# Kernel optimization log

Measured on AMD Instinct MI355X. Metric: run time of the kernel, lower is better.

The kernel has to match this reference:

```python
import jax, jax.numpy as jnp
import numpy as np

B, H, W, C = 32, 224, 224, 3
HID = 64


def setup_inputs() -> dict:
    key = jax.random.key(0)
    k0, k1, k2 = jax.random.split(key, 3)
    inputs = jax.random.normal(k0, (B, H, W, C), dtype=jnp.float32)
    # Localization-net dense params. Original uses zeros init (identity transform);
    # we use small random weights plus the identity affine bias so the sampling
    # grid is a nontrivial perturbation of identity.
    w1 = jax.random.normal(k1, (H * W * C, HID), dtype=jnp.float32) * 1e-3
    b1 = jnp.zeros((HID,), dtype=jnp.float32)
    w2 = jax.random.normal(k2, (HID, 6), dtype=jnp.float32) * 1e-2
    b2 = jnp.array([1.0, 0.0, 0.0, 0.0, 1.0, 0.0], dtype=jnp.float32)
    return {"inputs": inputs, "w1": w1, "b1": b1, "w2": w2, "b2": b2}


def _bilinear_sampler(img, x_s, y_s):
    # img: [B,H,W,C]; x_s, y_s: [B,H,W] normalized coords in [-1,1]
    Bn, Hn, Wn, Cn = img.shape
    x = 0.5 * (x_s + 1.0) * (Wn - 1)
    y = 0.5 * (y_s + 1.0) * (Hn - 1)
    x0 = jnp.floor(x).astype(jnp.int32)
    x1 = x0 + 1
    y0 = jnp.floor(y).astype(jnp.int32)
    y1 = y0 + 1
    x0c = jnp.clip(x0, 0, Wn - 1)
    x1c = jnp.clip(x1, 0, Wn - 1)
    y0c = jnp.clip(y0, 0, Hn - 1)
    y1c = jnp.clip(y1, 0, Hn - 1)
    b_idx = jnp.arange(Bn, dtype=jnp.int32)[:, None, None]
    Ia = img[b_idx, y0c, x0c]  # [B,H,W,C]
    Ib = img[b_idx, y1c, x0c]
    Ic = img[b_idx, y0c, x1c]
    Id = img[b_idx, y1c, x1c]
    x0f = x0c.astype(x.dtype)
    x1f = x1c.astype(x.dtype)
    y0f = y0c.astype(y.dtype)
    y1f = y1c.astype(y.dtype)
    wa = ((x1f - x) * (y1f - y))[..., None]
    wb = ((x1f - x) * (y - y0f))[..., None]
    wc = ((x - x0f) * (y1f - y))[..., None]
    wd = ((x - x0f) * (y - y0f))[..., None]
    return wa * Ia + wb * Ib + wc * Ic + wd * Id


def reference(inputs, w1, b1, w2, b2):
    Bn, Hn, Wn, Cn = inputs.shape
    # NOTE: original keras code overwrites the conv branch with flatten(inputs),
    # so the conv/maxpool layers are dead code and omitted. Dropout is identity
    # at inference (training=False).
    flat = inputs.reshape(Bn, -1)
    h = jnp.tanh(flat @ w1 + b1)
    theta = jnp.tanh(h @ w2 + b2).reshape(Bn, 2, 3)
    # affine sampling grid over normalized target coords
    xt, yt = jnp.meshgrid(
        jnp.linspace(-1.0, 1.0, Wn, dtype=inputs.dtype),
        jnp.linspace(-1.0, 1.0, Hn, dtype=inputs.dtype),
    )  # each [H,W]
    grid = jnp.stack([xt.ravel(), yt.ravel(), jnp.ones_like(xt).ravel()])  # [3,H*W]
    batch_grid = jnp.einsum("bij,jk->bik", theta, grid).reshape(Bn, 2, Hn, Wn)
    x_s = batch_grid[:, 0]
    y_s = batch_grid[:, 1]
    return _bilinear_sampler(inputs, x_s, y_s)
```

## Files before the change

### kernel.cpp

```cpp
#include <hip/hip_runtime.h>

#define BATCH 32
#define HDIM 224
#define WDIM 224
#define CDIM 3
#define KTOT (HDIM * WDIM * CDIM)
#define HID 64
#define KCHUNK 256
#define NBLK1 (KTOT / KCHUNK)
#define PIX (HDIM * WDIM)
#define BLK3 49

__global__ __launch_bounds__(256, 4) void k1_gemm(const float* __restrict__ flat,
                                                  const float* __restrict__ w1,
                                                  float* __restrict__ part) {
    __shared__ float smem[8192];
    const int tid  = threadIdx.x;
    const int lane = tid & 63;
    const int wave = tid >> 6;
    const int k0   = blockIdx.x * KCHUNK;
    const int kw   = wave * 64;

    float w[64];
    const float* wp = w1 + (size_t)(k0 + kw) * HID + lane;
#pragma unroll
    for (int i = 0; i < 64; ++i)
        w[i] = wp[(size_t)i * HID];

#pragma unroll
    for (int t = 0; t < 8; ++t) {
        const int idx = tid + t * 256;
        const int b   = idx >> 6;
        const int kq  = idx & 63;
        *(float4*)(smem + b * 256 + kq * 4) =
            *(const float4*)(flat + (size_t)b * KTOT + k0 + kq * 4);
    }
    __syncthreads();

    float acc[32];
#pragma unroll
    for (int j = 0; j < 32; ++j) acc[j] = 0.0f;

#pragma unroll
    for (int kk = 0; kk < 64; kk += 4) {
#pragma unroll
        for (int b = 0; b < 32; ++b) {
            const float4 x = *(const float4*)(smem + b * 256 + kw + kk);
            float a = acc[b];
            a = fmaf(x.x, w[kk + 0], a);
            a = fmaf(x.y, w[kk + 1], a);
            a = fmaf(x.z, w[kk + 2], a);
            a = fmaf(x.w, w[kk + 3], a);
            acc[b] = a;
        }
    }
    __syncthreads();

#pragma unroll
    for (int j = 0; j < 32; ++j)
        smem[wave * 2048 + j * 64 + lane] = acc[j];
    __syncthreads();

    float* po = part + (size_t)blockIdx.x * 2048;
#pragma unroll
    for (int t = 0; t < 8; ++t) {
        const int idx = tid + t * 256;
        po[idx] = smem[idx] + smem[2048 + idx] +
                  smem[4096 + idx] + smem[6144 + idx];
    }
}

__global__ __launch_bounds__(256) void k1_reduce(const float* __restrict__ part,
                                                 float* __restrict__ hacc) {
    __shared__ float red[256];
    const int tid    = threadIdx.x;
    const int o      = tid & 31;
    const int g      = tid >> 5;
    const int o_base = blockIdx.x * 32;

    float s = 0.0f;
    for (int blk = g; blk < NBLK1; blk += 8)
        s += part[(size_t)blk * 2048 + o_base + o];
    red[tid] = s;
    __syncthreads();
    if (g == 0) {
        float t = 0.0f;
#pragma unroll
        for (int gg = 0; gg < 8; ++gg)
            t += red[gg * 32 + o];
        hacc[o_base + o] = t;
    }
}

__global__ __launch_bounds__(256) void k3_sample(const float* __restrict__ img,
                                                 const float* __restrict__ hacc,
                                                 const float* __restrict__ b1,
                                                 const float* __restrict__ w2,
                                                 const float* __restrict__ b2,
                                                 float* __restrict__ out) {
    const int b     = blockIdx.x / BLK3;
    const int strip = blockIdx.x - b * BLK3;
    const int tid   = threadIdx.x;

    __shared__ float sh[HID];
    __shared__ float sth[6];
    if (tid < HID)
        sh[tid] = tanhf(hacc[b * HID + tid] + b1[tid]);
    __syncthreads();
    if (tid < 6) {
        float s = b2[tid];
#pragma unroll
        for (int t = 0; t < HID; ++t)
            s = fmaf(sh[t], w2[t * 6 + tid], s);
        sth[tid] = tanhf(s);
    }
    __syncthreads();

    const float t0 = sth[0], t1 = sth[1], t2 = sth[2];
    const float t3 = sth[3], t4 = sth[4], t5 = sth[5];

    const float* base = img + (size_t)b * KTOT;
    const int pix0 = strip * 1024 + tid * 4;

    float res[12];
#pragma unroll
    for (int p = 0; p < 4; ++p) {
        const int pix = pix0 + p;
        const int i = pix / WDIM;
        const int j = pix - i * WDIM;

        const float xt = (2.0f * (float)j - (float)(WDIM - 1)) / (float)(WDIM - 1);
        const float yt = (2.0f * (float)i - (float)(HDIM - 1)) / (float)(HDIM - 1);

        const float xs = t0 * xt + t1 * yt + t2;
        const float ys = t3 * xt + t4 * yt + t5;

        const float x = 0.5f * (xs + 1.0f) * (float)(WDIM - 1);
        const float y = 0.5f * (ys + 1.0f) * (float)(HDIM - 1);

        const int x0 = (int)floorf(x);
        const int y0 = (int)floorf(y);

        const int x0c = min(max(x0, 0), WDIM - 1);
        const int x1c = min(max(x0 + 1, 0), WDIM - 1);
        const int y0c = min(max(y0, 0), HDIM - 1);
        const int y1c = min(max(y0 + 1, 0), HDIM - 1);

        const float x0f = (float)x0c, x1f = (float)x1c;
        const float y0f = (float)y0c, y1f = (float)y1c;

        const float wa = (x1f - x) * (y1f - y);
        const float wb = (x1f - x) * (y - y0f);
        const float wc = (x - x0f) * (y1f - y);
        const float wd = (x - x0f) * (y - y0f);

        const float* pa = base + (size_t)(y0c * WDIM + x0c) * 3;
        const float* pb = base + (size_t)(y1c * WDIM + x0c) * 3;
        const float* pc = base + (size_t)(y0c * WDIM + x1c) * 3;
        const float* pd = base + (size_t)(y1c * WDIM + x1c) * 3;

#pragma unroll
        for (int c = 0; c < 3; ++c)
            res[p * 3 + c] = wa * pa[c] + wb * pb[c] + wc * pc[c] + wd * pd[c];
    }

    float4* po = (float4*)(out + (size_t)b * KTOT + (size_t)pix0 * 3);
    po[0] = make_float4(res[0], res[1], res[2],  res[3]);
    po[1] = make_float4(res[4], res[5], res[6],  res[7]);
    po[2] = make_float4(res[8], res[9], res[10], res[11]);
}

extern "C" void kernel_launch(void* const* d_in, const int* in_sizes, int n_in,
                              void* d_out, int out_size, void* d_ws, size_t ws_size,
                              hipStream_t stream) {
    const float* inputs = (const float*)d_in[0];
    const float* w1     = (const float*)d_in[1];
    const float* b1     = (const float*)d_in[2];
    const float* w2     = (const float*)d_in[3];
    const float* b2     = (const float*)d_in[4];
    float* out = (float*)d_out;

    float* part = (float*)d_ws;
    float* hacc = part + (size_t)NBLK1 * 2048;

    k1_gemm<<<NBLK1, 256, 0, stream>>>(inputs, w1, part);
    k1_reduce<<<HID * BATCH / 32, 256, 0, stream>>>(part, hacc);
    k3_sample<<<BATCH * BLK3, 256, 0, stream>>>(inputs, hacc, b1, w2, b2, out);
}
```

Measured before the change: 152.1 us.

## Restructure localization GEMM into per-thread batch×hidden tiles with smaller K chunks

```diff
diff --git a/kernel.cpp b/kernel.cpp
--- a/kernel.cpp
+++ b/kernel.cpp
@@ -6,68 +6,73 @@
 #define CDIM 3
 #define KTOT (HDIM * WDIM * CDIM)
 #define HID 64
-#define KCHUNK 256
-#define NBLK1 (KTOT / KCHUNK)
+#define KC 128
+#define NBLK1 (KTOT / KC)
 #define PIX (HDIM * WDIM)
 #define BLK3 49
 
 __global__ __launch_bounds__(256, 4) void k1_gemm(const float* __restrict__ flat,
                                                   const float* __restrict__ w1,
                                                   float* __restrict__ part) {
-    __shared__ float smem[8192];
+    __shared__ float smem[BATCH * KC];
     const int tid  = threadIdx.x;
     const int lane = tid & 63;
     const int wave = tid >> 6;
-    const int k0   = blockIdx.x * KCHUNK;
-    const int kw   = wave * 64;
-
-    float w[64];
-    const float* wp = w1 + (size_t)(k0 + kw) * HID + lane;
-#pragma unroll
-    for (int i = 0; i < 64; ++i)
-        w[i] = wp[(size_t)i * HID];
+    const int h4   = lane & 15;
+    const int bq   = lane >> 4;
+    const int b0   = wave * 8 + bq * 2;
+    const int k0   = blockIdx.x * KC;
 
 #pragma unroll
-    for (int t = 0; t < 8; ++t) {
+    for (int t = 0; t < 4; ++t) {
         const int idx = tid + t * 256;
-        const int b   = idx >> 6;
-        const int kq  = idx & 63;
-        *(float4*)(smem + b * 256 + kq * 4) =
+        const int b   = idx >> 5;
+        const int kq  = idx & 31;
+        *(float4*)(&smem[b * KC + kq * 4]) =
             *(const float4*)(flat + (size_t)b * KTOT + k0 + kq * 4);
     }
     __syncthreads();
 
-    float acc[32];
+    float4 acc[2];
+    acc[0] = make_float4(0.f, 0.f, 0.f, 0.f);
+    acc[1] = make_float4(0.f, 0.f, 0.f, 0.f);
+
+    for (int p = 0; p < 8; ++p) {
+        const int kp = p * 16;
+
+        float4 wr[16];
 #pragma unroll
-    for (int j = 0; j < 32; ++j) acc[j] = 0.0f;
+        for (int s = 0; s < 4; ++s) {
+            const int sp = ((s + bq) & 3) * 4;
+#pragma unroll
+            for (int j = 0; j < 4; ++j)
+                wr[s * 4 + j] = *(const float4*)(
+                    w1 + (size_t)(k0 + kp + sp + j) * HID + h4 * 4);
+        }
 
 #pragma unroll
-    for (int kk = 0; kk < 64; kk += 4) {
+        for (int s = 0; s < 4; ++s) {
+            const int sp = ((s + bq) & 3) * 4;
 #pragma unroll
-        for (int b = 0; b < 32; ++b) {
-            const float4 x = *(const float4*)(smem + b * 256 + kw + kk);
-            float a = acc[b];
-            a = fmaf(x.x, w[kk + 0], a);
-            a = fmaf(x.y, w[kk + 1], a);
-            a = fmaf(x.z, w[kk + 2], a);
-            a = fmaf(x.w, w[kk + 3], a);
-            acc[b] = a;
+            for (int b = 0; b < 2; ++b) {
+                const float4 x = *(const float4*)(&smem[(b0 + b) * KC + kp + sp]);
+                const float xs[4] = {x.x, x.y, x.z, x.w};
+                float* A = (float*)&acc[b];
+#pragma unroll
+                for (int j = 0; j < 4; ++j) {
+                    const float* wf = (const float*)&wr[s * 4 + j];
+#pragma unroll
+                    for (int c = 0; c < 4; ++c)
+                        A[c] = fmaf(xs[j], wf[c], A[c]);
+                }
+            }
         }
     }
-    __syncthreads();
-
-#pragma unroll
-    for (int j = 0; j < 32; ++j)
-        smem[wave * 2048 + j * 64 + lane] = acc[j];
-    __syncthreads();
 
     float* po = part + (size_t)blockIdx.x * 2048;
 #pragma unroll
-    for (int t = 0; t < 8; ++t) {
-        const int idx = tid + t * 256;
-        po[idx] = smem[idx] + smem[2048 + idx] +
-                  smem[4096 + idx] + smem[6144 + idx];
-    }
+    for (int b = 0; b < 2; ++b)
+        *(float4*)(po + (b0 + b) * HID + h4 * 4) = acc[b];
 }
 
 __global__ __launch_bounds__(256) void k1_reduce(const float* __restrict__ part,
```

Measured after the change: 182.7 us. +20.1%, slower.
